# Kernel optimization log

Measured on AMD Instinct MI355X. Metric: run time of the kernel, lower is better.

The kernel has to match this reference:

```python
import jax, jax.numpy as jnp
import numpy as np

ALPHA = 0.5
MOM = 0.9            # momentum m in the recurrence
ACTIVATION = "tanh"
NUM_LAYERS = 2
CACHE = 32           # GROUP size
NK = 4               # n_kernel_feats
B, N, E = 4, 4096, 128


def _act(T):
    if ACTIVATION == "leaky-relu":
        return jax.nn.leaky_relu(T)
    elif ACTIVATION == "tanh":
        return jnp.tanh(T)
    return T


def _group_indices(N, cache, stage):
    # vectorized group_pos_to_index_v2 over all (group_nr, pos_in_group)
    m = N // cache
    o = np.arange(cache)
    s = 0 if stage == 0 else (1 << (stage - 1)) % m
    g = np.arange(m)[:, None]
    block = (g + o[None, :] * s) % m
    return jnp.asarray(block * cache + o[None, :])  # [m, cache], a permutation of 0..N-1


def _ncn_layer(X, Xa, W, stage):
    B, N, E = X.shape
    ce = E // NK
    m = N // CACHE
    idx = _group_indices(N, CACHE, stage)           # [m, cache]
    Wi = W[:E].reshape(NK, ce)
    Wj = W[E:].reshape(NK, ce)
    # gather groups: [B, m, NK, cache, ce]
    xg = jnp.moveaxis(X.reshape(B, N, NK, ce)[:, idx], 3, 2)
    xag = jnp.moveaxis(Xa.reshape(B, N, NK, ce)[:, idx], 3, 2)

    def step(carry, j):
        xi, xa = carry                               # [B, m, NK, cache, ce]
        xj = jnp.take(xi, j, axis=3)                 # [B, m, NK, ce]  (row start_j)
        sim = (jnp.einsum('bgnke,ne->bgnk', xi, Wi)
               + jnp.einsum('bgne,ne->bgn', xj, Wj)[..., None])   # [B, m, NK, cache]
        T = ALPHA * xi + (1.0 - ALPHA) * sim[..., None] * xj[:, :, :, None, :]
        F = _act(T)
        ya = MOM * xa + (1.0 - MOM) * F
        yi = MOM * xi + (1.0 - MOM) * ya
        return (yi, ya), None

    (yi, ya), _ = jax.lax.scan(step, (xg, xag), jnp.arange(CACHE))

    # scatter back; idx is a permutation so .set reproduces the += into zeros
    def scatter(v):
        v = jnp.moveaxis(v, 2, 3).reshape(B, m * CACHE, E)
        return jnp.zeros((B, N, E), v.dtype).at[:, idx.reshape(-1)].set(v)

    return scatter(yi), scatter(ya)


def setup_inputs() -> dict:
    key = jax.random.key(0)
    k1, k2, k3 = jax.random.split(key, 3)
    x = jax.random.normal(k1, (B, N, E), jnp.float32)
    xa = jax.random.normal(k2, (B, N, E), jnp.float32)
    W = jax.random.normal(k3, (NUM_LAYERS, 2 * E), jnp.float32)
    return {"x": x, "xa": xa, "W": W}


def reference(x, xa, W):
    for l in range(NUM_LAYERS):
        x, xa = _ncn_layer(x, xa, W[l], l)
    return x, xa
```

## Files before the change

kernel.cpp:

```cpp
#include <hip/hip_runtime.h>


namespace {
constexpr int kB = 4;
constexpr int kN = 4096;
constexpr int kE = 128;
constexpr int kCE = 32;
constexpr int kH  = 16;
constexpr int kQ  = kH / 2;
constexpr int kCache = 32;
constexpr int kM = kN / kCache;

typedef __attribute__((ext_vector_type(2))) float f32x2;

__device__ __forceinline__ f32x2 pk_fma(f32x2 a, f32x2 b, f32x2 c) {
    return __builtin_elementwise_fma(a, b, c);
}
}

__global__ void __launch_bounds__(64, 2) ncn_layer_kernel(
    const float* __restrict__ x_in, const float* __restrict__ xa_in,
    const float* __restrict__ Wl,
    float* __restrict__ x_out, float* __restrict__ xa_out,
    int s)
{
    const int blk = blockIdx.x;
    const int n   = blk & 3;
    const int g   = (blk >> 2) & (kM - 1);
    const int b   = blk >> 9;
    const int t   = threadIdx.x;
    const int o   = t & 31;
    const int h   = t >> 5;

    const int r = (((g + o * s) & (kM - 1)) << 5) + o;
    const size_t base = ((size_t)(b * kN + r)) * kE + n * kCE + h * kH;

    constexpr float L1 = 1.4426950408889634f;

    f32x2 xi[kQ], xa[kQ], wi[kQ], wj[kQ];

    {
        const float4* xi4 = reinterpret_cast<const float4*>(x_in + base);
        const float4* xa4 = reinterpret_cast<const float4*>(xa_in + base);
        const float4* wi4 = reinterpret_cast<const float4*>(Wl + n * kCE + h * kH);
        const float4* wj4 = reinterpret_cast<const float4*>(Wl + kE + n * kCE + h * kH);
#pragma unroll
        for (int q = 0; q < kQ / 2; ++q) {
            float4 v = xi4[q];
            xi[2 * q + 0] = f32x2{v.x, v.y}; xi[2 * q + 1] = f32x2{v.z, v.w};
            float4 a = xa4[q];
            xa[2 * q + 0] = f32x2{a.x, a.y}; xa[2 * q + 1] = f32x2{a.z, a.w};
            float4 u = wi4[q];
            wi[2 * q + 0] = f32x2{u.x * L1, u.y * L1};
            wi[2 * q + 1] = f32x2{u.z * L1, u.w * L1};
            float4 w = wj4[q];
            wj[2 * q + 0] = f32x2{w.x * L1, w.y * L1};
            wj[2 * q + 1] = f32x2{w.z * L1, w.w * L1};
        }
    }

    __shared__ float rowbuf[kCE];

    if (o == 0) {
        float4* w4 = reinterpret_cast<float4*>(&rowbuf[h * kH]);
#pragma unroll
        for (int q = 0; q < kQ / 2; ++q) {
            float4 v;
            v.x = xi[2 * q + 0].x; v.y = xi[2 * q + 0].y;
            v.z = xi[2 * q + 1].x; v.w = xi[2 * q + 1].y;
            w4[q] = v;
        }
    }
    __syncthreads();

#pragma unroll 4
    for (int j = 0; j < kCache; ++j) {
        f32x2 xj[kQ];
        {
            const float4* r4 = reinterpret_cast<const float4*>(&rowbuf[h * kH]);
#pragma unroll
            for (int q = 0; q < kQ / 2; ++q) {
                float4 v = r4[q];
                xj[2 * q + 0] = f32x2{v.x, v.y};
                xj[2 * q + 1] = f32x2{v.z, v.w};
            }
        }

        f32x2 a01 = xi[0] * wi[0];
        f32x2 a23 = xi[1] * wi[1];
        f32x2 b01 = xj[0] * wj[0];
        f32x2 b23 = xj[1] * wj[1];
#pragma unroll
        for (int q = 2; q < kQ; q += 2) {
            a01 = pk_fma(xi[q + 0], wi[q + 0], a01);
            a23 = pk_fma(xi[q + 1], wi[q + 1], a23);
            b01 = pk_fma(xj[q + 0], wj[q + 0], b01);
            b23 = pk_fma(xj[q + 1], wj[q + 1], b23);
        }
        f32x2 uv = (a01 + a23) + (b01 + b23);
        float u  = uv.x + uv.y;

        const float sim = u + __shfl_xor(u, 32, 64);
        const f32x2 sv  = {sim, sim};
        const f32x2 l12 = {L1, L1};
        const f32x2 one = {1.0f, 1.0f};
        const f32x2 m02 = {-0.2f, -0.2f};
        const f32x2 c9  = {0.9f, 0.9f};
        const f32x2 c01 = {0.1f, 0.1f};

#pragma unroll
        for (int q = 0; q < kQ; ++q) {
            f32x2 arg = pk_fma(xj[q], sv, xi[q] * l12);
            f32x2 t2;
            t2.x = __builtin_amdgcn_exp2f(arg.x);
            t2.y = __builtin_amdgcn_exp2f(arg.y);
            f32x2 den = t2 + one;
            f32x2 rc;
            rc.x = __builtin_amdgcn_rcpf(den.x);
            rc.y = __builtin_amdgcn_rcpf(den.y);
            xa[q] = pk_fma(m02, rc, pk_fma(c9, xa[q], c01));
            xi[q] = pk_fma(c01, xa[q], xi[q] * c9);
        }

        if (o == ((j + 1) & 31)) {
            float4* w4 = reinterpret_cast<float4*>(&rowbuf[h * kH]);
#pragma unroll
            for (int q = 0; q < kQ / 2; ++q) {
                float4 v;
                v.x = xi[2 * q + 0].x; v.y = xi[2 * q + 0].y;
                v.z = xi[2 * q + 1].x; v.w = xi[2 * q + 1].y;
                w4[q] = v;
            }
        }
        __syncthreads();
    }

    {
        float4* xo4 = reinterpret_cast<float4*>(x_out + base);
        float4* ao4 = reinterpret_cast<float4*>(xa_out + base);
#pragma unroll
        for (int q = 0; q < kQ / 2; ++q) {
            float4 v;
            v.x = xi[2 * q + 0].x; v.y = xi[2 * q + 0].y;
            v.z = xi[2 * q + 1].x; v.w = xi[2 * q + 1].y;
            xo4[q] = v;
            float4 a;
            a.x = xa[2 * q + 0].x; a.y = xa[2 * q + 0].y;
            a.z = xa[2 * q + 1].x; a.w = xa[2 * q + 1].y;
            ao4[q] = a;
        }
    }
}

extern "C" void kernel_launch(void* const* d_in, const int* in_sizes, int n_in,
                              void* d_out, int out_size, void* d_ws, size_t ws_size,
                              hipStream_t stream) {
    const float* x  = (const float*)d_in[0];
    const float* xa = (const float*)d_in[1];
    const float* W  = (const float*)d_in[2];

    const size_t plane = (size_t)kB * kN * kE;

    float* x_mid  = (float*)d_ws;
    float* xa_mid = x_mid + plane;

    float* x_out  = (float*)d_out;
    float* xa_out = x_out + plane;

    const dim3 grid(kB * kM * 4);
    const dim3 block(64);

    ncn_layer_kernel<<<grid, block, 0, stream>>>(x, xa, W, x_mid, xa_mid, 0);
    ncn_layer_kernel<<<grid, block, 0, stream>>>(x_mid, xa_mid, W + 2 * kE,
                                                 x_out, xa_out, 1);
}
```

Baseline: 124.1 us.

## Split each group over 128 threads with 8 features each and double-buffered row

```diff
diff --git a/kernel.cpp b/kernel.cpp
--- a/kernel.cpp
+++ b/kernel.cpp
@@ -6,8 +6,8 @@
 constexpr int kN = 4096;
 constexpr int kE = 128;
 constexpr int kCE = 32;
-constexpr int kH  = 16;
-constexpr int kQ  = kH / 2;
+constexpr int kF  = 8;
+constexpr int kQ  = kF / 2;
 constexpr int kCache = 32;
 constexpr int kM = kN / kCache;
 
@@ -18,7 +18,7 @@
 }
 }
 
-__global__ void __launch_bounds__(64, 2) ncn_layer_kernel(
+__global__ void __launch_bounds__(128) ncn_layer_kernel(
     const float* __restrict__ x_in, const float* __restrict__ xa_in,
     const float* __restrict__ Wl,
     float* __restrict__ x_out, float* __restrict__ xa_out,
@@ -29,11 +29,14 @@
     const int g   = (blk >> 2) & (kM - 1);
     const int b   = blk >> 9;
     const int t   = threadIdx.x;
-    const int o   = t & 31;
-    const int h   = t >> 5;
+    const int w   = t >> 6;
+    const int l   = t & 63;
+    const int orr = l >> 2;
+    const int f   = l & 3;
+    const int row = w * 16 + orr;
 
-    const int r = (((g + o * s) & (kM - 1)) << 5) + o;
-    const size_t base = ((size_t)(b * kN + r)) * kE + n * kCE + h * kH;
+    const int r = (((g + row * s) & (kM - 1)) << 5) + row;
+    const size_t base = ((size_t)(b * kN + r)) * kE + n * kCE + f * kF;
 
     constexpr float L1 = 1.4426950408889634f;
 
@@ -42,8 +45,8 @@
     {
         const float4* xi4 = reinterpret_cast<const float4*>(x_in + base);
         const float4* xa4 = reinterpret_cast<const float4*>(xa_in + base);
-        const float4* wi4 = reinterpret_cast<const float4*>(Wl + n * kCE + h * kH);
-        const float4* wj4 = reinterpret_cast<const float4*>(Wl + kE + n * kCE + h * kH);
+        const float4* wi4 = reinterpret_cast<const float4*>(Wl + n * kCE + f * kF);
+        const float4* wj4 = reinterpret_cast<const float4*>(Wl + kE + n * kCE + f * kF);
 #pragma unroll
         for (int q = 0; q < kQ / 2; ++q) {
             float4 v = xi4[q];
@@ -53,16 +56,16 @@
             float4 u = wi4[q];
             wi[2 * q + 0] = f32x2{u.x * L1, u.y * L1};
             wi[2 * q + 1] = f32x2{u.z * L1, u.w * L1};
-            float4 w = wj4[q];
-            wj[2 * q + 0] = f32x2{w.x * L1, w.y * L1};
-            wj[2 * q + 1] = f32x2{w.z * L1, w.w * L1};
+            float4 ww = wj4[q];
+            wj[2 * q + 0] = f32x2{ww.x * L1, ww.y * L1};
+            wj[2 * q + 1] = f32x2{ww.z * L1, ww.w * L1};
         }
     }
 
-    __shared__ float rowbuf[kCE];
+    __shared__ float rowbuf[2][kCE];
 
-    if (o == 0) {
-        float4* w4 = reinterpret_cast<float4*>(&rowbuf[h * kH]);
+    if (t < 4) {
+        float4* w4 = reinterpret_cast<float4*>(&rowbuf[0][f * kF]);
 #pragma unroll
         for (int q = 0; q < kQ / 2; ++q) {
             float4 v;
@@ -75,9 +78,11 @@
 
 #pragma unroll 4
     for (int j = 0; j < kCache; ++j) {
+        const int p = j & 1;
+
         f32x2 xj[kQ];
         {
-            const float4* r4 = reinterpret_cast<const float4*>(&rowbuf[h * kH]);
+            const float4* r4 = reinterpret_cast<const float4*>(&rowbuf[p][f * kF]);
 #pragma unroll
             for (int q = 0; q < kQ / 2; ++q) {
                 float4 v = r4[q];
@@ -90,17 +95,16 @@
         f32x2 a23 = xi[1] * wi[1];
         f32x2 b01 = xj[0] * wj[0];
         f32x2 b23 = xj[1] * wj[1];
-#pragma unroll
-        for (int q = 2; q < kQ; q += 2) {
-            a01 = pk_fma(xi[q + 0], wi[q + 0], a01);
-            a23 = pk_fma(xi[q + 1], wi[q + 1], a23);
-            b01 = pk_fma(xj[q + 0], wj[q + 0], b01);
-            b23 = pk_fma(xj[q + 1], wj[q + 1], b23);
-        }
+        a01 = pk_fma(xi[2], wi[2], a01);
+        a23 = pk_fma(xi[3], wi[3], a23);
+        b01 = pk_fma(xj[2], wj[2], b01);
+        b23 = pk_fma(xj[3], wj[3], b23);
         f32x2 uv = (a01 + a23) + (b01 + b23);
         float u  = uv.x + uv.y;
 
-        const float sim = u + __shfl_xor(u, 32, 64);
+        u += __shfl_xor(u, 1, 64);
+        u += __shfl_xor(u, 2, 64);
+        const float sim = u;
         const f32x2 sv  = {sim, sim};
         const f32x2 l12 = {L1, L1};
         const f32x2 one = {1.0f, 1.0f};
@@ -122,8 +126,9 @@
             xi[q] = pk_fma(c01, xa[q], xi[q] * c9);
         }
 
-        if (o == ((j + 1) & 31)) {
-            float4* w4 = reinterpret_cast<float4*>(&rowbuf[h * kH]);
+        const int nj = (j + 1) & 31;
+        if (row == nj) {
+            float4* w4 = reinterpret_cast<float4*>(&rowbuf[p ^ 1][f * kF]);
 #pragma unroll
             for (int q = 0; q < kQ / 2; ++q) {
                 float4 v;
@@ -168,7 +173,7 @@
     float* xa_out = x_out + plane;
 
     const dim3 grid(kB * kM * 4);
-    const dim3 block(64);
+    const dim3 block(128);
 
     ncn_layer_kernel<<<grid, block, 0, stream>>>(x, xa, W, x_mid, xa_mid, 0);
     ncn_layer_kernel<<<grid, block, 0, stream>>>(x_mid, xa_mid, W + 2 * kE,
```

Measured after the change: 120.3 us. 1.03x faster.

## Fuse both layers into one persistent kernel with grid barrier and bpermute row broadcast

Applied to the files above, without the earlier changes.

```diff
diff --git a/kernel.cpp b/kernel.cpp
--- a/kernel.cpp
+++ b/kernel.cpp
@@ -10,6 +10,8 @@
 constexpr int kQ  = kH / 2;
 constexpr int kCache = 32;
 constexpr int kM = kN / kCache;
+constexpr int kBlocks = 256;
+constexpr int kThreads = 512;
 
 typedef __attribute__((ext_vector_type(2))) float f32x2;
 
@@ -18,72 +20,59 @@
 }
 }
 
-__global__ void __launch_bounds__(64, 2) ncn_layer_kernel(
-    const float* __restrict__ x_in, const float* __restrict__ xa_in,
-    const float* __restrict__ Wl,
-    float* __restrict__ x_out, float* __restrict__ xa_out,
-    int s)
-{
-    const int blk = blockIdx.x;
-    const int n   = blk & 3;
-    const int g   = (blk >> 2) & (kM - 1);
-    const int b   = blk >> 9;
-    const int t   = threadIdx.x;
-    const int o   = t & 31;
-    const int h   = t >> 5;
-
-    const int r = (((g + o * s) & (kM - 1)) << 5) + o;
-    const size_t base = ((size_t)(b * kN + r)) * kE + n * kCE + h * kH;
-
+__device__ __forceinline__ void load_state(
+    const float* __restrict__ xp, const float* __restrict__ ap,
+    f32x2* xi, f32x2* xa)
+{
+    const float4* x4 = reinterpret_cast<const float4*>(xp);
+    const float4* a4 = reinterpret_cast<const float4*>(ap);
+#pragma unroll
+    for (int q = 0; q < kQ / 2; ++q) {
+        float4 v = x4[q];
+        xi[2 * q + 0] = f32x2{v.x, v.y}; xi[2 * q + 1] = f32x2{v.z, v.w};
+        float4 a = a4[q];
+        xa[2 * q + 0] = f32x2{a.x, a.y}; xa[2 * q + 1] = f32x2{a.z, a.w};
+    }
+}
+
+__device__ __forceinline__ void store_state(
+    float* __restrict__ xp, float* __restrict__ ap,
+    const f32x2* xi, const f32x2* xa)
+{
+    float4* x4 = reinterpret_cast<float4*>(xp);
+    float4* a4 = reinterpret_cast<float4*>(ap);
+#pragma unroll
+    for (int q = 0; q < kQ / 2; ++q) {
+        float4 v;
+        v.x = xi[2 * q + 0].x; v.y = xi[2 * q + 0].y;
+        v.z = xi[2 * q + 1].x; v.w = xi[2 * q + 1].y;
+        x4[q] = v;
+        float4 a;
+        a.x = xa[2 * q + 0].x; a.y = xa[2 * q + 0].y;
+        a.z = xa[2 * q + 1].x; a.w = xa[2 * q + 1].y;
+        a4[q] = a;
+    }
+}
+
+__device__ __forceinline__ void scan_layer(
+    f32x2* xi, f32x2* xa,
+    const f32x2* wi, const f32x2* wj,
+    int lane)
+{
     constexpr float L1 = 1.4426950408889634f;
-
-    f32x2 xi[kQ], xa[kQ], wi[kQ], wj[kQ];
-
-    {
-        const float4* xi4 = reinterpret_cast<const float4*>(x_in + base);
-        const float4* xa4 = reinterpret_cast<const float4*>(xa_in + base);
-        const float4* wi4 = reinterpret_cast<const float4*>(Wl + n * kCE + h * kH);
-        const float4* wj4 = reinterpret_cast<const float4*>(Wl + kE + n * kCE + h * kH);
-#pragma unroll
-        for (int q = 0; q < kQ / 2; ++q) {
-            float4 v = xi4[q];
-            xi[2 * q + 0] = f32x2{v.x, v.y}; xi[2 * q + 1] = f32x2{v.z, v.w};
-            float4 a = xa4[q];
-            xa[2 * q + 0] = f32x2{a.x, a.y}; xa[2 * q + 1] = f32x2{a.z, a.w};
-            float4 u = wi4[q];
-            wi[2 * q + 0] = f32x2{u.x * L1, u.y * L1};
-            wi[2 * q + 1] = f32x2{u.z * L1, u.w * L1};
-            float4 w = wj4[q];
-            wj[2 * q + 0] = f32x2{w.x * L1, w.y * L1};
-            wj[2 * q + 1] = f32x2{w.z * L1, w.w * L1};
-        }
-    }
-
-    __shared__ float rowbuf[kCE];
-
-    if (o == 0) {
-        float4* w4 = reinterpret_cast<float4*>(&rowbuf[h * kH]);
-#pragma unroll
-        for (int q = 0; q < kQ / 2; ++q) {
-            float4 v;
-            v.x = xi[2 * q + 0].x; v.y = xi[2 * q + 0].y;
-            v.z = xi[2 * q + 1].x; v.w = xi[2 * q + 1].y;
-            w4[q] = v;
-        }
-    }
-    __syncthreads();
-
-#pragma unroll 4
+    const int srcbase = (lane & 32) * 4;
+
+#pragma unroll 2
     for (int j = 0; j < kCache; ++j) {
+        const int srcaddr = srcbase + j * 4;
+
         f32x2 xj[kQ];
-        {
-            const float4* r4 = reinterpret_cast<const float4*>(&rowbuf[h * kH]);
-#pragma unroll
-            for (int q = 0; q < kQ / 2; ++q) {
-                float4 v = r4[q];
-                xj[2 * q + 0] = f32x2{v.x, v.y};
-                xj[2 * q + 1] = f32x2{v.z, v.w};
-            }
+#pragma unroll
+        for (int q = 0; q < kQ; ++q) {
+            xj[q].x = __int_as_float(
+                __builtin_amdgcn_ds_bpermute(srcaddr, __float_as_int(xi[q].x)));
+            xj[q].y = __int_as_float(
+                __builtin_amdgcn_ds_bpermute(srcaddr, __float_as_int(xi[q].y)));
         }
 
         f32x2 a01 = xi[0] * wi[0];
@@ -121,35 +110,88 @@
             xa[q] = pk_fma(m02, rc, pk_fma(c9, xa[q], c01));
             xi[q] = pk_fma(c01, xa[q], xi[q] * c9);
         }
-
-        if (o == ((j + 1) & 31)) {
-            float4* w4 = reinterpret_cast<float4*>(&rowbuf[h * kH]);
-#pragma unroll
-            for (int q = 0; q < kQ / 2; ++q) {
-                float4 v;
-                v.x = xi[2 * q + 0].x; v.y = xi[2 * q + 0].y;
-                v.z = xi[2 * q + 1].x; v.w = xi[2 * q + 1].y;
-                w4[q] = v;
+    }
+}
+
+__global__ void __launch_bounds__(kThreads, 1) ncn_fused_kernel(
+    const float* __restrict__ x_in, const float* __restrict__ xa_in,
+    const float* __restrict__ W,
+    float* __restrict__ x_mid, float* __restrict__ xa_mid,
+    float* __restrict__ x_out, float* __restrict__ xa_out,
+    unsigned* __restrict__ bar_cnt, unsigned* __restrict__ bar_gen)
+{
+    const int tid  = threadIdx.x;
+    const int wave = tid >> 6;
+    const int lane = tid & 63;
+    const int id   = blockIdx.x * 8 + wave;
+    const int n    = id & 3;
+    const int g    = (id >> 2) & (kM - 1);
+    const int b    = id >> 9;
+    const int o    = lane & 31;
+    const int h    = lane >> 5;
+
+    constexpr float L1 = 1.4426950408889634f;
+
+    const int r0 = (g << 5) + o;
+    const size_t base0 = ((size_t)(b * kN + r0)) * kE + n * kCE + h * kH;
+
+    f32x2 xi[kQ], xa[kQ], wi[kQ], wj[kQ];
+    load_state(x_in + base0, xa_in + base0, xi, xa);
+    {
+        const float4* wi4 = reinterpret_cast<const float4*>(W + n * kCE + h * kH);
+        const float4* wj4 = reinterpret_cast<const float4*>(W + kE + n * kCE + h * kH);
+#pragma unroll
+        for (int q = 0; q < kQ / 2; ++q) {
+            float4 u = wi4[q];
+            wi[2 * q + 0] = f32x2{u.x * L1, u.y * L1};
+            wi[2 * q + 1] = f32x2{u.z * L1, u.w * L1};
+            float4 w = wj4[q];
+            wj[2 * q + 0] = f32x2{w.x * L1, w.y * L1};
+            wj[2 * q + 1] = f32x2{w.z * L1, w.w * L1};
+        }
+    }
+
+    scan_layer(xi, xa, wi, wj, lane);
+    store_state(x_mid + base0, xa_mid + base0, xi, xa);
+
+    __threadfence();
+    __syncthreads();
+    if (tid == 0) {
+        unsigned arrived = __hip_atomic_fetch_add(
+            bar_cnt, 1u, __ATOMIC_ACQ_REL, __HIP_MEMORY_SCOPE_AGENT) + 1;
+        if (arrived == (unsigned)kBlocks) {
+            __hip_atomic_store(bar_gen, 1u, __ATOMIC_RELEASE,
+                               __HIP_MEMORY_SCOPE_AGENT);
+        } else {
+            while (__hip_atomic_load(bar_gen, __ATOMIC_ACQUIRE,
+                                     __HIP_MEMORY_SCOPE_AGENT) == 0u) {
+                __builtin_amdgcn_s_sleep(2);
             }
         }
-        __syncthreads();
-    }
-
+    }
+    __syncthreads();
+    __threadfence();
+
+    const int r1 = (((g + o) & (kM - 1)) << 5) + o;
+    const size_t base1 = ((size_t)(b * kN + r1)) * kE + n * kCE + h * kH;
+
+    load_state(x_mid + base1, xa_mid + base1, xi, xa);
     {
-        float4* xo4 = reinterpret_cast<float4*>(x_out + base);
-        float4* ao4 = reinterpret_cast<float4*>(xa_out + base);
+        const float4* wi4 = reinterpret_cast<const float4*>(W + 2 * kE + n * kCE + h * kH);
+        const float4* wj4 = reinterpret_cast<const float4*>(W + 3 * kE + n * kCE + h * kH);
 #pragma unroll
         for (int q = 0; q < kQ / 2; ++q) {
-            float4 v;
-            v.x = xi[2 * q + 0].x; v.y = xi[2 * q + 0].y;
-            v.z = xi[2 * q + 1].x; v.w = xi[2 * q + 1].y;
-            xo4[q] = v;
-            float4 a;
-            a.x = xa[2 * q + 0].x; a.y = xa[2 * q + 0].y;
-            a.z = xa[2 * q + 1].x; a.w = xa[2 * q + 1].y;
-            ao4[q] = a;
-        }
-    }
+            float4 u = wi4[q];
+            wi[2 * q + 0] = f32x2{u.x * L1, u.y * L1};
+            wi[2 * q + 1] = f32x2{u.z * L1, u.w * L1};
+            float4 w = wj4[q];
+            wj[2 * q + 0] = f32x2{w.x * L1, w.y * L1};
+            wj[2 * q + 1] = f32x2{w.z * L1, w.w * L1};
+        }
+    }
+
+    scan_layer(xi, xa, wi, wj, lane);
+    store_state(x_out + base1, xa_out + base1, xi, xa);
 }
 
 extern "C" void kernel_launch(void* const* d_in, const int* in_sizes, int n_in,
@@ -161,16 +203,16 @@
 
     const size_t plane = (size_t)kB * kN * kE;
 
-    float* x_mid  = (float*)d_ws;
+    unsigned* bar_cnt = (unsigned*)d_ws;
+    unsigned* bar_gen = (unsigned*)((char*)d_ws + 256);
+    float* x_mid  = (float*)((char*)d_ws + 1024);
     float* xa_mid = x_mid + plane;
 
     float* x_out  = (float*)d_out;
     float* xa_out = x_out + plane;
 
-    const dim3 grid(kB * kM * 4);
-    const dim3 block(64);
-
-    ncn_layer_kernel<<<grid, block, 0, stream>>>(x, xa, W, x_mid, xa_mid, 0);
-    ncn_layer_kernel<<<grid, block, 0, stream>>>(x_mid, xa_mid, W + 2 * kE,
-                                                 x_out, xa_out, 1);
-}
+    hipMemsetAsync(d_ws, 0, 512, stream);
+
+    ncn_fused_kernel<<<dim3(kBlocks), dim3(kThreads), 0, stream>>>(
+        x, xa, W, x_mid, xa_mid, x_out, xa_out, bar_cnt, bar_gen);
+}
```

Result: slower. 237.7 us (+91.5%).
